# Kernel optimization log

Measured on AMD Instinct MI355X. Metric: run time of the kernel, lower is better.

## Reference

```python
import jax, jax.numpy as jnp
import numpy as np

DIM = 1024
N_QUAT = DIM // 4
LN_EPS = 1e-5
NORM_EPS = 1e-12


def quat_mul(q1, q2):
    # q1, q2: [B, L, N, 4]
    r1, i1, j1, k1 = q1[..., 0], q1[..., 1], q1[..., 2], q1[..., 3]
    r2, i2, j2, k2 = q2[..., 0], q2[..., 1], q2[..., 2], q2[..., 3]
    r = r1 * r2 - i1 * i2 - j1 * j2 - k1 * k2
    i = r1 * i2 + i1 * r2 + j1 * k2 - k1 * j2
    j = r1 * j2 - i1 * k2 + j1 * r2 + k1 * i2
    k = r1 * k2 + i1 * j2 - j1 * i2 + k1 * r2
    return jnp.stack([r, i, j, k], axis=-1)


def quat_conj(q):
    return q * jnp.array([1.0, -1.0, -1.0, -1.0], dtype=q.dtype)


def setup_inputs() -> dict:
    key = jax.random.key(0)
    ks = jax.random.split(key, 7)
    B, L, D = 4, 4096, DIM
    s = 1.0 / np.sqrt(D)
    return {
        "x": jax.random.normal(ks[0], (B, L, D), dtype=jnp.float32),
        "Wk": jax.random.normal(ks[1], (D, D), dtype=jnp.float32) * s,
        "bk": jnp.zeros((D,), dtype=jnp.float32),
        "Wv": jax.random.normal(ks[2], (D, D), dtype=jnp.float32) * s,
        "bv": jnp.zeros((D,), dtype=jnp.float32),
        "ln_g": jnp.ones((D,), dtype=jnp.float32),
        "ln_b": jnp.zeros((D,), dtype=jnp.float32),
        "Wo": jax.random.normal(ks[3], (D, D), dtype=jnp.float32) * s,
        "bo": jnp.zeros((D,), dtype=jnp.float32),
    }


def reference(x, Wk, bk, Wv, bv, ln_g, ln_b, Wo, bo):
    B, L, D = x.shape
    keys = (x @ Wk.T + bk).reshape(B, L, N_QUAT, 4)
    knorm = jnp.linalg.norm(keys, axis=-1, keepdims=True)
    keys = keys / jnp.maximum(knorm, NORM_EPS)  # F.normalize
    values = (x @ Wv.T + bv).reshape(B, L, N_QUAT, 4)
    bound = quat_mul(values, keys)
    memory = jnp.cumsum(bound, axis=1)
    retrieved = quat_mul(memory, quat_conj(keys)).reshape(B, L, D)
    positions = jnp.arange(1, L + 1, dtype=x.dtype)
    retrieved = retrieved / jnp.sqrt(positions)[None, :, None]
    # LayerNorm over last dim
    mu = jnp.mean(retrieved, axis=-1, keepdims=True)
    var = jnp.var(retrieved, axis=-1, keepdims=True)
    normed = (retrieved - mu) / jnp.sqrt(var + LN_EPS) * ln_g + ln_b
    return x + (normed @ Wo.T + bo)
```

## Files before the change

### kernel.cpp

```cpp
#include <hip/hip_runtime.h>
#include <cstdint>
#include <cstddef>


typedef float    f32x4 __attribute__((ext_vector_type(4)));
typedef _Float16 f16x8 __attribute__((ext_vector_type(8)));
typedef _Float16 f16x4 __attribute__((ext_vector_type(4)));

#define DEV static __device__ __forceinline__

constexpr int BATCH = 4;
constexpr int LSEQ  = 4096;
constexpr int DIMN  = 1024;
constexpr int MROW  = BATCH * LSEQ;
constexpr int SEG   = 128;
constexpr int SL    = LSEQ / SEG;
constexpr int NT    = DIMN / 64;

DEV f32x4 qmul(f32x4 a, f32x4 b) {
  f32x4 r;
  r.x = a.x*b.x - a.y*b.y - a.z*b.z - a.w*b.w;
  r.y = a.x*b.y + a.y*b.x + a.z*b.w - a.w*b.z;
  r.z = a.x*b.z - a.y*b.w + a.z*b.x + a.w*b.y;
  r.w = a.x*b.w + a.y*b.z - a.z*b.y + a.w*b.x;
  return r;
}

DEV f32x4 h2f(f16x4 h) {
  return (f32x4){(float)h.x, (float)h.y, (float)h.z, (float)h.w};
}

__global__ __launch_bounds__(256) void k_cast_all(
    const float* __restrict__ x, const float* __restrict__ w0,
    const float* __restrict__ w1, const float* __restrict__ w2,
    _Float16* __restrict__ out) {
  const int XN4 = MROW * DIMN / 4;
  const int WN4 = DIMN * DIMN / 4;
  int i = blockIdx.x * 256 + threadIdx.x;
  if (i >= XN4 + 3 * WN4) return;
  const float* src; int j;
  if (i < XN4)                { src = x;  j = i; }
  else if (i < XN4 + WN4)     { src = w0; j = i - XN4; }
  else if (i < XN4 + 2 * WN4) { src = w1; j = i - XN4 - WN4; }
  else                        { src = w2; j = i - XN4 - 2 * WN4; }
  f32x4 v = ((const f32x4*)src)[j];
  f16x4 o = { (_Float16)v.x, (_Float16)v.y, (_Float16)v.z, (_Float16)v.w };
  ((f16x4*)out)[i] = o;
}

__global__ __launch_bounds__(512, 2) void k_gemm256(
    const _Float16* __restrict__ A, const _Float16* __restrict__ Bw,
    const float* __restrict__ biasA, const float* __restrict__ biasB, int nsplit,
    _Float16* __restrict__ C, int ldC, int nbn) {
  extern __shared__ char smem[];
  const int tid  = threadIdx.x;
  const int lane = tid & 63;
  const int wid  = tid >> 6;
  const int wr = wid >> 2, wc = wid & 3;

  const int nwg = gridDim.x;
  const int cpx = nwg >> 3;
  const int swz = (blockIdx.x & 7) * cpx + (blockIdx.x >> 3);
  const int bm = swz / nbn, bn = swz % nbn;

  auto regBase = [](int slot, int isB, int half) -> unsigned {
    return (unsigned)(((slot * 2 + isB) * 2 + half) * 16384);
  };
  const int r8    = lane >> 3;
  const int sslot = (lane & 7) ^ r8;
  const char* aT = (const char*)(A  + (size_t)bm * 256 * DIMN);
  const char* bT = (const char*)(Bw + (size_t)bn * 256 * DIMN);

  auto stage = [&](int isB, int half, int slot, int kt) {
    const char* gb = (isB ? bT : aT) + (size_t)(half * 128) * 2048 + kt * 128;
    const unsigned reg = regBase(slot, isB, half);
#pragma unroll
    for (int i = 0; i < 2; ++i) {
      const int c = wid * 2 + i;
      const char* src = gb + (size_t)(c * 8 + r8) * 2048 + (sslot << 4);
      __builtin_amdgcn_global_load_lds(
          (const __attribute__((address_space(1))) void*)src,
          (__attribute__((address_space(3))) void*)(smem + reg + c * 1024), 16, 0, 0);
    }
  };
  auto fragA = [&](int slot, int m, int kk) -> f16x8 {
    const int half = m >> 2;
    const int row  = wr * 64 + (m & 3) * 16 + (lane & 15);
    const int sl   = (kk * 4 + (lane >> 4)) ^ (row & 7);
    return *(const f16x8*)(smem + regBase(slot, 0, half) + row * 128 + (sl << 4));
  };
  auto fragB = [&](int slot, int n, int kk) -> f16x8 {
    const int half = n >> 1;
    const int row  = wc * 32 + (n & 1) * 16 + (lane & 15);
    const int sl   = (kk * 4 + (lane >> 4)) ^ (row & 7);
    return *(const f16x8*)(smem + regBase(slot, 1, half) + row * 128 + (sl << 4));
  };

  f32x4 acc[8][4];
#pragma unroll
  for (int m = 0; m < 8; ++m)
#pragma unroll
    for (int n = 0; n < 4; ++n) acc[m][n] = (f32x4){0.f, 0.f, 0.f, 0.f};

  stage(0, 0, 0, 0); stage(0, 1, 0, 0); stage(1, 0, 0, 0); stage(1, 1, 0, 0);

  f16x8 a[4][2], b[4][2];
#pragma unroll 2
  for (int T = 0; T < NT; ++T) {
    const int slot = T & 1, ns = slot ^ 1;
    const bool pf = (T + 1 < NT);
    if (pf) {
      stage(0, 0, ns, T + 1); stage(0, 1, ns, T + 1);
      asm volatile("s_waitcnt vmcnt(4)" ::: "memory");
    } else {
      asm volatile("s_waitcnt vmcnt(0)" ::: "memory");
    }
    __builtin_amdgcn_s_barrier();

#pragma unroll
    for (int m = 0; m < 4; ++m) { a[m][0] = fragA(slot, m, 0); a[m][1] = fragA(slot, m, 1); }
#pragma unroll
    for (int n = 0; n < 4; ++n) { b[n][0] = fragB(slot, n, 0); b[n][1] = fragB(slot, n, 1); }
    __builtin_amdgcn_s_setprio(1);
#pragma unroll
    for (int m = 0; m < 4; ++m)
#pragma unroll
      for (int n = 0; n < 4; ++n) {
        acc[m][n] = __builtin_amdgcn_mfma_f32_16x16x32_f16(a[m][0], b[n][0], acc[m][n], 0, 0, 0);
        acc[m][n] = __builtin_amdgcn_mfma_f32_16x16x32_f16(a[m][1], b[n][1], acc[m][n], 0, 0, 0);
      }
    __builtin_amdgcn_s_setprio(0);

    if (pf) { stage(1, 0, ns, T + 1); stage(1, 1, ns, T + 1); }

#pragma unroll
    for (int m = 0; m < 4; ++m) { a[m][0] = fragA(slot, m + 4, 0); a[m][1] = fragA(slot, m + 4, 1); }
    __builtin_amdgcn_s_setprio(1);
#pragma unroll
    for (int m = 0; m < 4; ++m)
#pragma unroll
      for (int n = 0; n < 4; ++n) {
        acc[m + 4][n] = __builtin_amdgcn_mfma_f32_16x16x32_f16(a[m][0], b[n][0], acc[m + 4][n], 0, 0, 0);
        acc[m + 4][n] = __builtin_amdgcn_mfma_f32_16x16x32_f16(a[m][1], b[n][1], acc[m + 4][n], 0, 0, 0);
      }
    __builtin_amdgcn_s_setprio(0);
    __builtin_amdgcn_s_barrier();
  }

  const int r0 = bm * 256 + wr * 64 + ((lane >> 4) << 2);
  const int c0 = bn * 256 + wc * 32 + (lane & 15);
#pragma unroll
  for (int n = 0; n < 4; ++n) {
    const int col = c0 + (n >> 1) * 128 + (n & 1) * 16;
    const float bc = (col < nsplit) ? biasA[col] : biasB[col - nsplit];
#pragma unroll
    for (int m = 0; m < 8; ++m) {
      const int row = r0 + (m >> 2) * 128 + (m & 3) * 16;
#pragma unroll
      for (int t = 0; t < 4; ++t) {
        C[(size_t)(row + t) * ldC + col] = (_Float16)(acc[m][n][t] + bc);
      }
    }
  }
}

__global__ __launch_bounds__(512, 2) void k_gemm_out(
    const _Float16* __restrict__ A, const _Float16* __restrict__ Bw,
    const float* __restrict__ bias, const _Float16* __restrict__ residH,
    float* __restrict__ C, int nbn) {
  extern __shared__ char smem[];
  const int tid  = threadIdx.x;
  const int lane = tid & 63;
  const int wid  = tid >> 6;
  const int wr = wid >> 2, wc = wid & 3;

  const int nwg = gridDim.x;
  const int cpx = nwg >> 3;
  const int swz = (blockIdx.x & 7) * cpx + (blockIdx.x >> 3);
  const int bm = swz / nbn, bn = swz % nbn;

  const int r8    = lane >> 3;
  const int sslot = (lane & 7) ^ r8;
  const char* aT = (const char*)(A  + (size_t)bm * 128 * DIMN);
  const char* bT = (const char*)(Bw + (size_t)bn * 256 * DIMN);

  auto stage3 = [&](int slot, int kt) {
    char* base = smem + slot * 49152;
#pragma unroll
    for (int i = 0; i < 2; ++i) {
      const int c = wid * 2 + i;
      const char* src = aT + kt * 128 + (size_t)(c * 8 + r8) * 2048 + (sslot << 4);
      __builtin_amdgcn_global_load_lds(
          (const __attribute__((address_space(1))) void*)src,
          (__attribute__((address_space(3))) void*)(base + c * 1024), 16, 0, 0);
    }
#pragma unroll
    for (int i = 0; i < 4; ++i) {
      const int c = wid * 4 + i;
      const char* src = bT + kt * 128 + (size_t)(c * 8 + r8) * 2048 + (sslot << 4);
      __builtin_amdgcn_global_load_lds(
          (const __attribute__((address_space(1))) void*)src,
          (__attribute__((address_space(3))) void*)(base + 16384 + c * 1024), 16, 0, 0);
    }
  };
  auto fragA = [&](int slot, int m, int kk) -> f16x8 {
    const int row = wr * 64 + m * 16 + (lane & 15);
    const int sl  = (kk * 4 + (lane >> 4)) ^ (row & 7);
    return *(const f16x8*)(smem + slot * 49152 + row * 128 + (sl << 4));
  };
  auto fragB = [&](int slot, int n, int kk) -> f16x8 {
    const int row = (n >> 1) * 128 + wc * 32 + (n & 1) * 16 + (lane & 15);
    const int sl  = (kk * 4 + (lane >> 4)) ^ (row & 7);
    return *(const f16x8*)(smem + slot * 49152 + 16384 + row * 128 + (sl << 4));
  };

  f32x4 acc[4][4];
#pragma unroll
  for (int m = 0; m < 4; ++m)
#pragma unroll
    for (int n = 0; n < 4; ++n) acc[m][n] = (f32x4){0.f, 0.f, 0.f, 0.f};

  stage3(0, 0); stage3(1, 1);

  f16x8 a[4][2], b[4][2];
  int s = 0, sw = 2;
  for (int T = 0; T < NT; ++T) {
    if (T + 1 < NT) asm volatile("s_waitcnt vmcnt(6)" ::: "memory");
    else            asm volatile("s_waitcnt vmcnt(0)" ::: "memory");
    __builtin_amdgcn_s_barrier();
#pragma unroll
    for (int m = 0; m < 4; ++m) { a[m][0] = fragA(s, m, 0); a[m][1] = fragA(s, m, 1); }
#pragma unroll
    for (int n = 0; n < 4; ++n) { b[n][0] = fragB(s, n, 0); b[n][1] = fragB(s, n, 1); }
    if (T + 2 < NT) stage3(sw, T + 2);
    __builtin_amdgcn_s_setprio(1);
#pragma unroll
    for (int m = 0; m < 4; ++m)
#pragma unroll
      for (int n = 0; n < 4; ++n) {
        acc[m][n] = __builtin_amdgcn_mfma_f32_16x16x32_f16(a[m][0], b[n][0], acc[m][n], 0, 0, 0);
        acc[m][n] = __builtin_amdgcn_mfma_f32_16x16x32_f16(a[m][1], b[n][1], acc[m][n], 0, 0, 0);
      }
    __builtin_amdgcn_s_setprio(0);
    __builtin_amdgcn_s_barrier();
    s = (s == 2) ? 0 : s + 1;
    sw = (sw == 2) ? 0 : sw + 1;
  }

  const int r0 = bm * 128 + wr * 64 + ((lane >> 4) << 2);
  const int c0 = bn * 256 + wc * 32 + (lane & 15);
#pragma unroll
  for (int n = 0; n < 4; ++n) {
    const int col = c0 + (n >> 1) * 128 + (n & 1) * 16;
    const float bc = bias[col];
#pragma unroll
    for (int m = 0; m < 4; ++m) {
      const int row = r0 + m * 16;
#pragma unroll
      for (int t = 0; t < 4; ++t) {
        const size_t off = (size_t)(row + t) * DIMN + col;
        C[off] = acc[m][n][t] + bc + (float)residH[off];
      }
    }
  }
}

__global__ __launch_bounds__(256) void k_segsum(const _Float16* __restrict__ KVh,
                                                float* __restrict__ segsum) {
  const int b = blockIdx.x >> 7, seg = blockIdx.x & 127, n = threadIdx.x;
  f32x4 ssum = (f32x4){0.f, 0.f, 0.f, 0.f};
  const size_t rb = (size_t)(b * LSEQ + seg * SL) * 2048 + n * 4;
  for (int l = 0; l < SL; ++l) {
    const size_t p = rb + (size_t)l * 2048;
    f32x4 kq = h2f(*(const f16x4*)(KVh + p));
    f32x4 vq = h2f(*(const f16x4*)(KVh + p + 1024));
    float nn = sqrtf(kq.x*kq.x + kq.y*kq.y + kq.z*kq.z + kq.w*kq.w);
    f32x4 kh = kq * (1.0f / fmaxf(nn, 1e-12f));
    ssum += qmul(vq, kh);
  }
  ((f32x4*)segsum)[(size_t)blockIdx.x * 256 + n] = ssum;
}

__global__ __launch_bounds__(256) void k_retrieve_ln(
    const _Float16* __restrict__ KVh, const float* __restrict__ segsum,
    const float* __restrict__ g, const float* __restrict__ bb,
    _Float16* __restrict__ out) {
  const int b = blockIdx.x >> 7, seg = blockIdx.x & 127, n = threadIdx.x;
  const int wid = n >> 6, lane = n & 63;
  __shared__ float p1[2][4], p2[2][4];

  f32x4 m0 = (f32x4){0.f, 0.f, 0.f, 0.f}, m1 = (f32x4){0.f, 0.f, 0.f, 0.f};
  {
    const f32x4* ss = (const f32x4*)segsum + (size_t)b * SEG * 256 + n;
    int s = 0;
    for (; s + 2 <= seg; s += 2) {
      m0 += ss[(size_t)s * 256];
      m1 += ss[(size_t)(s + 1) * 256];
    }
    if (s < seg) m0 += ss[(size_t)s * 256];
  }
  f32x4 mem = m0 + m1;

  const f32x4 gg  = ((const f32x4*)g)[n];
  const f32x4 bvv = ((const f32x4*)bb)[n];
  const size_t rb = (size_t)(b * LSEQ + seg * SL) * 2048 + n * 4;
  const int grow = b * LSEQ + seg * SL;

  f16x4 kq = *(const f16x4*)(KVh + rb);
  f16x4 vq = *(const f16x4*)(KVh + rb + 1024);
  for (int l = 0; l < SL; ++l) {
    f16x4 kqn, vqn;
    if (l + 1 < SL) {
      kqn = *(const f16x4*)(KVh + rb + (size_t)(l + 1) * 2048);
      vqn = *(const f16x4*)(KVh + rb + (size_t)(l + 1) * 2048 + 1024);
    }
    f32x4 kf = h2f(kq), vf = h2f(vq);
    float nn = sqrtf(kf.x*kf.x + kf.y*kf.y + kf.z*kf.z + kf.w*kf.w);
    f32x4 kh = kf * (1.0f / fmaxf(nn, 1e-12f));
    mem += qmul(vf, kh);
    f32x4 kc = (f32x4){kh.x, -kh.y, -kh.z, -kh.w};
    f32x4 r = qmul(mem, kc);
    r *= rsqrtf((float)(seg * SL + l + 1));

    float s1 = r.x + r.y + r.z + r.w;
    float s2 = r.x*r.x + r.y*r.y + r.z*r.z + r.w*r.w;
#pragma unroll
    for (int off = 32; off > 0; off >>= 1) {
      s1 += __shfl_down(s1, off, 64);
      s2 += __shfl_down(s2, off, 64);
    }
    if (lane == 0) { p1[l & 1][wid] = s1; p2[l & 1][wid] = s2; }
    __syncthreads();
    const float ts1 = p1[l & 1][0] + p1[l & 1][1] + p1[l & 1][2] + p1[l & 1][3];
    const float ts2 = p2[l & 1][0] + p2[l & 1][1] + p2[l & 1][2] + p2[l & 1][3];
    const float mu = ts1 * (1.0f / 1024.0f);
    const float var = ts2 * (1.0f / 1024.0f) - mu * mu;
    const float rstd = rsqrtf(var + 1e-5f);
    f32x4 nv = (r - mu) * rstd * gg + bvv;
    f16x4 o = { (_Float16)nv.x, (_Float16)nv.y, (_Float16)nv.z, (_Float16)nv.w };
    ((f16x4*)out)[(size_t)(grow + l) * 256 + n] = o;
    kq = kqn; vq = vqn;
  }
}

extern "C" void kernel_launch(void* const* d_in, const int* in_sizes, int n_in,
                              void* d_out, int out_size, void* d_ws, size_t ws_size,
                              hipStream_t stream) {
  const float* x    = (const float*)d_in[0];
  const float* Wk   = (const float*)d_in[1];
  const float* bk   = (const float*)d_in[2];
  const float* Wv   = (const float*)d_in[3];
  const float* bv   = (const float*)d_in[4];
  const float* ln_g = (const float*)d_in[5];
  const float* ln_b = (const float*)d_in[6];
  const float* Wo   = (const float*)d_in[7];
  const float* bo   = (const float*)d_in[8];
  float* out = (float*)d_out;

  char* ws = (char*)d_ws;
  size_t off = 0;
  auto alloc = [&](size_t bytes) -> void* {
    void* p = ws + off;
    off += (bytes + 255) & ~(size_t)255;
    return p;
  };
  _Float16* xb   = (_Float16*)alloc((size_t)MROW * DIMN * 2);
  _Float16* wkvb = (_Float16*)alloc((size_t)3 * DIMN * DIMN * 2);
  _Float16* KVh  = (_Float16*)alloc((size_t)MROW * 2 * DIMN * 2);
  float* segsum  = (float*)alloc((size_t)BATCH * SEG * DIMN * 4);
  _Float16* nb   = (_Float16*)alloc((size_t)MROW * DIMN * 2);
  _Float16* wob  = wkvb + (size_t)2 * DIMN * DIMN;
  (void)off; (void)ws_size; (void)in_sizes; (void)n_in; (void)out_size;

  hipFuncSetAttribute((const void*)k_gemm256,
                      hipFuncAttributeMaxDynamicSharedMemorySize, 131072);
  hipFuncSetAttribute((const void*)k_gemm_out,
                      hipFuncAttributeMaxDynamicSharedMemorySize, 147456);

  const int castN4 = MROW * DIMN / 4 + 3 * DIMN * DIMN / 4;
  k_cast_all<<<(castN4 + 255) / 256, 256, 0, stream>>>(x, Wk, Wv, Wo, xb);

  k_gemm256<<<(MROW / 256) * (2048 / 256), 512, 131072, stream>>>(
      xb, wkvb, bk, bv, 1024, KVh, 2048, 2048 / 256);

  k_segsum<<<BATCH * SEG, 256, 0, stream>>>(KVh, segsum);
  k_retrieve_ln<<<BATCH * SEG, 256, 0, stream>>>(KVh, segsum, ln_g, ln_b, nb);

  k_gemm_out<<<(MROW / 128) * (DIMN / 256), 512, 147456, stream>>>(
      nb, wob, bo, xb, out, DIMN / 256);
}
```

Baseline: 209.7 us.

## Split GEMM inner loops into quadrant phases interleaving LDS reads, prefetch and MFMA

Both GEMM kernels now run each K tile in smaller MFMA phases over half of the B fragments, ping-ponging between bl and bh registers. LDS fragment reads and global prefetch stages are interleaved between phases, fenced by extra barriers and lgkmcnt waits. The aim is to overlap LDS and global latency with matrix-core work and to cut register pressure from holding all B fragments at once. The cost is more barriers per iteration, and a full vmcnt(0) drain inside the first kernel's loop may serialise the prefetch it was meant to hide.

```diff
diff --git a/kernel.cpp b/kernel.cpp
--- a/kernel.cpp
+++ b/kernel.cpp
@@ -103,45 +103,73 @@
     for (int n = 0; n < 4; ++n) acc[m][n] = (f32x4){0.f, 0.f, 0.f, 0.f};
 
   stage(0, 0, 0, 0); stage(0, 1, 0, 0); stage(1, 0, 0, 0); stage(1, 1, 0, 0);
-
-  f16x8 a[4][2], b[4][2];
+  asm volatile("s_waitcnt vmcnt(0)" ::: "memory");
+  __builtin_amdgcn_s_barrier();
+
+  f16x8 a[4][2], bl[2][2], bh[2][2];
 #pragma unroll 2
   for (int T = 0; T < NT; ++T) {
     const int slot = T & 1, ns = slot ^ 1;
     const bool pf = (T + 1 < NT);
-    if (pf) {
-      stage(0, 0, ns, T + 1); stage(0, 1, ns, T + 1);
-      asm volatile("s_waitcnt vmcnt(4)" ::: "memory");
-    } else {
-      asm volatile("s_waitcnt vmcnt(0)" ::: "memory");
-    }
-    __builtin_amdgcn_s_barrier();
 
 #pragma unroll
     for (int m = 0; m < 4; ++m) { a[m][0] = fragA(slot, m, 0); a[m][1] = fragA(slot, m, 1); }
 #pragma unroll
-    for (int n = 0; n < 4; ++n) { b[n][0] = fragB(slot, n, 0); b[n][1] = fragB(slot, n, 1); }
-    __builtin_amdgcn_s_setprio(1);
-#pragma unroll
-    for (int m = 0; m < 4; ++m)
-#pragma unroll
-      for (int n = 0; n < 4; ++n) {
-        acc[m][n] = __builtin_amdgcn_mfma_f32_16x16x32_f16(a[m][0], b[n][0], acc[m][n], 0, 0, 0);
-        acc[m][n] = __builtin_amdgcn_mfma_f32_16x16x32_f16(a[m][1], b[n][1], acc[m][n], 0, 0, 0);
-      }
-    __builtin_amdgcn_s_setprio(0);
-
+    for (int n = 0; n < 2; ++n) { bl[n][0] = fragB(slot, n, 0); bl[n][1] = fragB(slot, n, 1); }
+    if (pf) { stage(0, 0, ns, T + 1); stage(0, 1, ns, T + 1); }
+    __builtin_amdgcn_s_barrier();
+    asm volatile("s_waitcnt lgkmcnt(0)" ::: "memory");
+    __builtin_amdgcn_s_setprio(1);
+#pragma unroll
+    for (int m = 0; m < 4; ++m)
+#pragma unroll
+      for (int n = 0; n < 2; ++n) {
+        acc[m][n] = __builtin_amdgcn_mfma_f32_16x16x32_f16(a[m][0], bl[n][0], acc[m][n], 0, 0, 0);
+        acc[m][n] = __builtin_amdgcn_mfma_f32_16x16x32_f16(a[m][1], bl[n][1], acc[m][n], 0, 0, 0);
+      }
+    __builtin_amdgcn_s_setprio(0);
+    __builtin_amdgcn_s_barrier();
+
+#pragma unroll
+    for (int n = 0; n < 2; ++n) { bh[n][0] = fragB(slot, n + 2, 0); bh[n][1] = fragB(slot, n + 2, 1); }
     if (pf) { stage(1, 0, ns, T + 1); stage(1, 1, ns, T + 1); }
+    __builtin_amdgcn_s_barrier();
+    asm volatile("s_waitcnt lgkmcnt(0)" ::: "memory");
+    __builtin_amdgcn_s_setprio(1);
+#pragma unroll
+    for (int m = 0; m < 4; ++m)
+#pragma unroll
+      for (int n = 0; n < 2; ++n) {
+        acc[m][n + 2] = __builtin_amdgcn_mfma_f32_16x16x32_f16(a[m][0], bh[n][0], acc[m][n + 2], 0, 0, 0);
+        acc[m][n + 2] = __builtin_amdgcn_mfma_f32_16x16x32_f16(a[m][1], bh[n][1], acc[m][n + 2], 0, 0, 0);
+      }
+    __builtin_amdgcn_s_setprio(0);
+    __builtin_amdgcn_s_barrier();
 
 #pragma unroll
     for (int m = 0; m < 4; ++m) { a[m][0] = fragA(slot, m + 4, 0); a[m][1] = fragA(slot, m + 4, 1); }
-    __builtin_amdgcn_s_setprio(1);
-#pragma unroll
-    for (int m = 0; m < 4; ++m)
-#pragma unroll
-      for (int n = 0; n < 4; ++n) {
-        acc[m + 4][n] = __builtin_amdgcn_mfma_f32_16x16x32_f16(a[m][0], b[n][0], acc[m + 4][n], 0, 0, 0);
-        acc[m + 4][n] = __builtin_amdgcn_mfma_f32_16x16x32_f16(a[m][1], b[n][1], acc[m + 4][n], 0, 0, 0);
+    __builtin_amdgcn_s_barrier();
+    asm volatile("s_waitcnt lgkmcnt(0)" ::: "memory");
+    __builtin_amdgcn_s_setprio(1);
+#pragma unroll
+    for (int m = 0; m < 4; ++m)
+#pragma unroll
+      for (int n = 0; n < 2; ++n) {
+        acc[m + 4][n + 2] = __builtin_amdgcn_mfma_f32_16x16x32_f16(a[m][0], bh[n][0], acc[m + 4][n + 2], 0, 0, 0);
+        acc[m + 4][n + 2] = __builtin_amdgcn_mfma_f32_16x16x32_f16(a[m][1], bh[n][1], acc[m + 4][n + 2], 0, 0, 0);
+      }
+    __builtin_amdgcn_s_setprio(0);
+    __builtin_amdgcn_s_barrier();
+
+    asm volatile("s_waitcnt vmcnt(0)" ::: "memory");
+    __builtin_amdgcn_s_barrier();
+    __builtin_amdgcn_s_setprio(1);
+#pragma unroll
+    for (int m = 0; m < 4; ++m)
+#pragma unroll
+      for (int n = 0; n < 2; ++n) {
+        acc[m + 4][n] = __builtin_amdgcn_mfma_f32_16x16x32_f16(a[m][0], bl[n][0], acc[m + 4][n], 0, 0, 0);
+        acc[m + 4][n] = __builtin_amdgcn_mfma_f32_16x16x32_f16(a[m][1], bl[n][1], acc[m + 4][n], 0, 0, 0);
       }
     __builtin_amdgcn_s_setprio(0);
     __builtin_amdgcn_s_barrier();
@@ -221,25 +249,42 @@
     for (int n = 0; n < 4; ++n) acc[m][n] = (f32x4){0.f, 0.f, 0.f, 0.f};
 
   stage3(0, 0); stage3(1, 1);
-
-  f16x8 a[4][2], b[4][2];
+  asm volatile("s_waitcnt vmcnt(6)" ::: "memory");
+  __builtin_amdgcn_s_barrier();
+
+  f16x8 a[4][2], bl[2][2], bh[2][2];
   int s = 0, sw = 2;
   for (int T = 0; T < NT; ++T) {
-    if (T + 1 < NT) asm volatile("s_waitcnt vmcnt(6)" ::: "memory");
+#pragma unroll
+    for (int m = 0; m < 4; ++m) { a[m][0] = fragA(s, m, 0); a[m][1] = fragA(s, m, 1); }
+#pragma unroll
+    for (int n = 0; n < 2; ++n) { bl[n][0] = fragB(s, n, 0); bl[n][1] = fragB(s, n, 1); }
+    if (T + 2 < NT) stage3(sw, T + 2);
+    __builtin_amdgcn_s_barrier();
+    asm volatile("s_waitcnt lgkmcnt(0)" ::: "memory");
+    __builtin_amdgcn_s_setprio(1);
+#pragma unroll
+    for (int m = 0; m < 4; ++m)
+#pragma unroll
+      for (int n = 0; n < 2; ++n) {
+        acc[m][n] = __builtin_amdgcn_mfma_f32_16x16x32_f16(a[m][0], bl[n][0], acc[m][n], 0, 0, 0);
+        acc[m][n] = __builtin_amdgcn_mfma_f32_16x16x32_f16(a[m][1], bl[n][1], acc[m][n], 0, 0, 0);
+      }
+    __builtin_amdgcn_s_setprio(0);
+    __builtin_amdgcn_s_barrier();
+#pragma unroll
+    for (int n = 0; n < 2; ++n) { bh[n][0] = fragB(s, n + 2, 0); bh[n][1] = fragB(s, n + 2, 1); }
+    if (T + 2 < NT) asm volatile("s_waitcnt vmcnt(6)" ::: "memory");
     else            asm volatile("s_waitcnt vmcnt(0)" ::: "memory");
     __builtin_amdgcn_s_barrier();
-#pragma unroll
-    for (int m = 0; m < 4; ++m) { a[m][0] = fragA(s, m, 0); a[m][1] = fragA(s, m, 1); }
-#pragma unroll
-    for (int n = 0; n < 4; ++n) { b[n][0] = fragB(s, n, 0); b[n][1] = fragB(s, n, 1); }
-    if (T + 2 < NT) stage3(sw, T + 2);
-    __builtin_amdgcn_s_setprio(1);
-#pragma unroll
-    for (int m = 0; m < 4; ++m)
-#pragma unroll
-      for (int n = 0; n < 4; ++n) {
-        acc[m][n] = __builtin_amdgcn_mfma_f32_16x16x32_f16(a[m][0], b[n][0], acc[m][n], 0, 0, 0);
-        acc[m][n] = __builtin_amdgcn_mfma_f32_16x16x32_f16(a[m][1], b[n][1], acc[m][n], 0, 0, 0);
+    asm volatile("s_waitcnt lgkmcnt(0)" ::: "memory");
+    __builtin_amdgcn_s_setprio(1);
+#pragma unroll
+    for (int m = 0; m < 4; ++m)
+#pragma unroll
+      for (int n = 0; n < 2; ++n) {
+        acc[m][n + 2] = __builtin_amdgcn_mfma_f32_16x16x32_f16(a[m][0], bh[n][0], acc[m][n + 2], 0, 0, 0);
+        acc[m][n + 2] = __builtin_amdgcn_mfma_f32_16x16x32_f16(a[m][1], bh[n][1], acc[m][n + 2], 0, 0, 0);
       }
     __builtin_amdgcn_s_setprio(0);
     __builtin_amdgcn_s_barrier();
```

Result: no change. 210.2 us (+0.3%).

## Fuse x fp16 cast into KV GEMM and use 256x256 tiles for output GEMM

Applied to the files above, without the earlier changes.

The KV projection GEMM now reads x in fp32 straight from global memory into registers, converts to fp16 and writes the swizzled tile to LDS itself. This removes the separate cast pass over x and its fp16 copy, and the output GEMM adds the fp32 residual x directly. The output GEMM moves from a 128x256 triple-buffered tile to a 256x256 double-buffered tile, and both GEMMs now interleave A-fragment loads with MFMAs in smaller chunks. In exchange, A staging uses registers and explicit LDS writes instead of direct global-to-LDS loads. The output GEMM also waits on all loads each iteration, which may expose memory latency.

```diff
diff --git a/kernel.cpp b/kernel.cpp
--- a/kernel.cpp
+++ b/kernel.cpp
@@ -30,28 +30,32 @@
   return (f32x4){(float)h.x, (float)h.y, (float)h.z, (float)h.w};
 }
 
-__global__ __launch_bounds__(256) void k_cast_all(
-    const float* __restrict__ x, const float* __restrict__ w0,
-    const float* __restrict__ w1, const float* __restrict__ w2,
-    _Float16* __restrict__ out) {
-  const int XN4 = MROW * DIMN / 4;
+DEV f16x8 cvt8(f32x4 lo, f32x4 hi) {
+  f16x8 r;
+  r[0] = (_Float16)lo.x; r[1] = (_Float16)lo.y; r[2] = (_Float16)lo.z; r[3] = (_Float16)lo.w;
+  r[4] = (_Float16)hi.x; r[5] = (_Float16)hi.y; r[6] = (_Float16)hi.z; r[7] = (_Float16)hi.w;
+  return r;
+}
+
+__global__ __launch_bounds__(256) void k_cast_w(
+    const float* __restrict__ w0, const float* __restrict__ w1,
+    const float* __restrict__ w2, _Float16* __restrict__ out) {
   const int WN4 = DIMN * DIMN / 4;
   int i = blockIdx.x * 256 + threadIdx.x;
-  if (i >= XN4 + 3 * WN4) return;
+  if (i >= 3 * WN4) return;
   const float* src; int j;
-  if (i < XN4)                { src = x;  j = i; }
-  else if (i < XN4 + WN4)     { src = w0; j = i - XN4; }
-  else if (i < XN4 + 2 * WN4) { src = w1; j = i - XN4 - WN4; }
-  else                        { src = w2; j = i - XN4 - 2 * WN4; }
+  if (i < WN4)          { src = w0; j = i; }
+  else if (i < 2 * WN4) { src = w1; j = i - WN4; }
+  else                  { src = w2; j = i - 2 * WN4; }
   f32x4 v = ((const f32x4*)src)[j];
   f16x4 o = { (_Float16)v.x, (_Float16)v.y, (_Float16)v.z, (_Float16)v.w };
   ((f16x4*)out)[i] = o;
 }
 
-__global__ __launch_bounds__(512, 2) void k_gemm256(
-    const _Float16* __restrict__ A, const _Float16* __restrict__ Bw,
-    const float* __restrict__ biasA, const float* __restrict__ biasB, int nsplit,
-    _Float16* __restrict__ C, int ldC, int nbn) {
+__global__ __launch_bounds__(512, 2) void k_gemm_kv(
+    const float* __restrict__ X, const _Float16* __restrict__ Bw,
+    const float* __restrict__ biasA, const float* __restrict__ biasB,
+    _Float16* __restrict__ C) {
   extern __shared__ char smem[];
   const int tid  = threadIdx.x;
   const int lane = tid & 63;
@@ -61,19 +65,19 @@
   const int nwg = gridDim.x;
   const int cpx = nwg >> 3;
   const int swz = (blockIdx.x & 7) * cpx + (blockIdx.x >> 3);
-  const int bm = swz / nbn, bn = swz % nbn;
+  const int bm = swz >> 3, bn = swz & 7;
+
+  const int r8    = lane >> 3;
+  const int sslot = (lane & 7) ^ r8;
+  const float* aX = X + (size_t)bm * 256 * DIMN;
+  const char* bT  = (const char*)(Bw + (size_t)bn * 256 * DIMN);
 
   auto regBase = [](int slot, int isB, int half) -> unsigned {
     return (unsigned)(((slot * 2 + isB) * 2 + half) * 16384);
   };
-  const int r8    = lane >> 3;
-  const int sslot = (lane & 7) ^ r8;
-  const char* aT = (const char*)(A  + (size_t)bm * 256 * DIMN);
-  const char* bT = (const char*)(Bw + (size_t)bn * 256 * DIMN);
-
-  auto stage = [&](int isB, int half, int slot, int kt) {
-    const char* gb = (isB ? bT : aT) + (size_t)(half * 128) * 2048 + kt * 128;
-    const unsigned reg = regBase(slot, isB, half);
+  auto stageB = [&](int half, int slot, int kt) {
+    const char* gb = bT + (size_t)(half * 128) * 2048 + kt * 128;
+    const unsigned reg = regBase(slot, 1, half);
 #pragma unroll
     for (int i = 0; i < 2; ++i) {
       const int c = wid * 2 + i;
@@ -83,6 +87,27 @@
           (__attribute__((address_space(3))) void*)(smem + reg + c * 1024), 16, 0, 0);
     }
   };
+  f32x4 areg[4][2];
+  auto loadA = [&](int kt) {
+#pragma unroll
+    for (int h = 0; h < 2; ++h)
+#pragma unroll
+      for (int i = 0; i < 2; ++i) {
+        const size_t ad = (size_t)(h * 128 + (wid * 2 + i) * 8 + r8) * DIMN
+                        + kt * 64 + sslot * 8;
+        areg[h * 2 + i][0] = *(const f32x4*)(aX + ad);
+        areg[h * 2 + i][1] = *(const f32x4*)(aX + ad + 4);
+      }
+  };
+  auto writeA = [&](int slot) {
+#pragma unroll
+    for (int h = 0; h < 2; ++h)
+#pragma unroll
+      for (int i = 0; i < 2; ++i) {
+        f16x8 v = cvt8(areg[h * 2 + i][0], areg[h * 2 + i][1]);
+        *(f16x8*)(smem + regBase(slot, 0, h) + (wid * 2 + i) * 1024 + lane * 16) = v;
+      }
+  };
   auto fragA = [&](int slot, int m, int kk) -> f16x8 {
     const int half = m >> 2;
     const int row  = wr * 64 + (m & 3) * 16 + (lane & 15);
@@ -102,49 +127,50 @@
 #pragma unroll
     for (int n = 0; n < 4; ++n) acc[m][n] = (f32x4){0.f, 0.f, 0.f, 0.f};
 
-  stage(0, 0, 0, 0); stage(0, 1, 0, 0); stage(1, 0, 0, 0); stage(1, 1, 0, 0);
-
-  f16x8 a[4][2], b[4][2];
+  loadA(0);
+  stageB(0, 0, 0); stageB(1, 0, 0);
+  asm volatile("s_waitcnt vmcnt(4)" ::: "memory");
+  __builtin_amdgcn_sched_barrier(0);
+  writeA(0);
+
 #pragma unroll 2
   for (int T = 0; T < NT; ++T) {
     const int slot = T & 1, ns = slot ^ 1;
     const bool pf = (T + 1 < NT);
     if (pf) {
-      stage(0, 0, ns, T + 1); stage(0, 1, ns, T + 1);
-      asm volatile("s_waitcnt vmcnt(4)" ::: "memory");
+      loadA(T + 1);
+      asm volatile("s_waitcnt vmcnt(8)" ::: "memory");
     } else {
       asm volatile("s_waitcnt vmcnt(0)" ::: "memory");
     }
+    asm volatile("s_waitcnt lgkmcnt(0)" ::: "memory");
     __builtin_amdgcn_s_barrier();
 
-#pragma unroll
-    for (int m = 0; m < 4; ++m) { a[m][0] = fragA(slot, m, 0); a[m][1] = fragA(slot, m, 1); }
+    f16x8 b[4][2], a2[2][2];
 #pragma unroll
     for (int n = 0; n < 4; ++n) { b[n][0] = fragB(slot, n, 0); b[n][1] = fragB(slot, n, 1); }
-    __builtin_amdgcn_s_setprio(1);
-#pragma unroll
-    for (int m = 0; m < 4; ++m)
-#pragma unroll
-      for (int n = 0; n < 4; ++n) {
-        acc[m][n] = __builtin_amdgcn_mfma_f32_16x16x32_f16(a[m][0], b[n][0], acc[m][n], 0, 0, 0);
-        acc[m][n] = __builtin_amdgcn_mfma_f32_16x16x32_f16(a[m][1], b[n][1], acc[m][n], 0, 0, 0);
-      }
-    __builtin_amdgcn_s_setprio(0);
-
-    if (pf) { stage(1, 0, ns, T + 1); stage(1, 1, ns, T + 1); }
-
-#pragma unroll
-    for (int m = 0; m < 4; ++m) { a[m][0] = fragA(slot, m + 4, 0); a[m][1] = fragA(slot, m + 4, 1); }
-    __builtin_amdgcn_s_setprio(1);
-#pragma unroll
-    for (int m = 0; m < 4; ++m)
-#pragma unroll
-      for (int n = 0; n < 4; ++n) {
-        acc[m + 4][n] = __builtin_amdgcn_mfma_f32_16x16x32_f16(a[m][0], b[n][0], acc[m + 4][n], 0, 0, 0);
-        acc[m + 4][n] = __builtin_amdgcn_mfma_f32_16x16x32_f16(a[m][1], b[n][1], acc[m + 4][n], 0, 0, 0);
-      }
-    __builtin_amdgcn_s_setprio(0);
-    __builtin_amdgcn_s_barrier();
+    if (pf) { stageB(0, ns, T + 1); stageB(1, ns, T + 1); }
+
+#pragma unroll
+    for (int mh = 0; mh < 4; ++mh) {
+      a2[0][0] = fragA(slot, mh * 2, 0);     a2[0][1] = fragA(slot, mh * 2, 1);
+      a2[1][0] = fragA(slot, mh * 2 + 1, 0); a2[1][1] = fragA(slot, mh * 2 + 1, 1);
+      __builtin_amdgcn_s_setprio(1);
+#pragma unroll
+      for (int mm = 0; mm < 2; ++mm)
+#pragma unroll
+        for (int n = 0; n < 4; ++n) {
+          acc[mh*2+mm][n] = __builtin_amdgcn_mfma_f32_16x16x32_f16(a2[mm][0], b[n][0], acc[mh*2+mm][n], 0, 0, 0);
+          acc[mh*2+mm][n] = __builtin_amdgcn_mfma_f32_16x16x32_f16(a2[mm][1], b[n][1], acc[mh*2+mm][n], 0, 0, 0);
+        }
+      __builtin_amdgcn_s_setprio(0);
+    }
+
+    if (pf) {
+      asm volatile("s_waitcnt vmcnt(4)" ::: "memory");
+      __builtin_amdgcn_sched_barrier(0);
+      writeA(ns);
+    }
   }
 
   const int r0 = bm * 256 + wr * 64 + ((lane >> 4) << 2);
@@ -152,13 +178,13 @@
 #pragma unroll
   for (int n = 0; n < 4; ++n) {
     const int col = c0 + (n >> 1) * 128 + (n & 1) * 16;
-    const float bc = (col < nsplit) ? biasA[col] : biasB[col - nsplit];
+    const float bc = (col < DIMN) ? biasA[col] : biasB[col - DIMN];
 #pragma unroll
     for (int m = 0; m < 8; ++m) {
       const int row = r0 + (m >> 2) * 128 + (m & 3) * 16;
 #pragma unroll
       for (int t = 0; t < 4; ++t) {
-        C[(size_t)(row + t) * ldC + col] = (_Float16)(acc[m][n][t] + bc);
+        C[(size_t)(row + t) * 2048 + col] = (_Float16)(acc[m][n][t] + bc);
       }
     }
   }
@@ -166,8 +192,8 @@
 
 __global__ __launch_bounds__(512, 2) void k_gemm_out(
     const _Float16* __restrict__ A, const _Float16* __restrict__ Bw,
-    const float* __restrict__ bias, const _Float16* __restrict__ residH,
-    float* __restrict__ C, int nbn) {
+    const float* __restrict__ bias, const float* __restrict__ resid,
+    float* __restrict__ C) {
   extern __shared__ char smem[];
   const int tid  = threadIdx.x;
   const int lane = tid & 63;
@@ -177,89 +203,92 @@
   const int nwg = gridDim.x;
   const int cpx = nwg >> 3;
   const int swz = (blockIdx.x & 7) * cpx + (blockIdx.x >> 3);
-  const int bm = swz / nbn, bn = swz % nbn;
+  const int bm = swz >> 2, bn = swz & 3;
 
   const int r8    = lane >> 3;
   const int sslot = (lane & 7) ^ r8;
-  const char* aT = (const char*)(A  + (size_t)bm * 128 * DIMN);
+  const char* aT = (const char*)(A  + (size_t)bm * 256 * DIMN);
   const char* bT = (const char*)(Bw + (size_t)bn * 256 * DIMN);
 
-  auto stage3 = [&](int slot, int kt) {
-    char* base = smem + slot * 49152;
+  auto regBase = [](int slot, int isB, int half) -> unsigned {
+    return (unsigned)(((slot * 2 + isB) * 2 + half) * 16384);
+  };
+  auto stage = [&](int isB, int half, int slot, int kt) {
+    const char* gb = (isB ? bT : aT) + (size_t)(half * 128) * 2048 + kt * 128;
+    const unsigned reg = regBase(slot, isB, half);
 #pragma unroll
     for (int i = 0; i < 2; ++i) {
       const int c = wid * 2 + i;
-      const char* src = aT + kt * 128 + (size_t)(c * 8 + r8) * 2048 + (sslot << 4);
+      const char* src = gb + (size_t)(c * 8 + r8) * 2048 + (sslot << 4);
       __builtin_amdgcn_global_load_lds(
           (const __attribute__((address_space(1))) void*)src,
-          (__attribute__((address_space(3))) void*)(base + c * 1024), 16, 0, 0);
-    }
-#pragma unroll
-    for (int i = 0; i < 4; ++i) {
-      const int c = wid * 4 + i;
-      const char* src = bT + kt * 128 + (size_t)(c * 8 + r8) * 2048 + (sslot << 4);
-      __builtin_amdgcn_global_load_lds(
-          (const __attribute__((address_space(1))) void*)src,
-          (__attribute__((address_space(3))) void*)(base + 16384 + c * 1024), 16, 0, 0);
+          (__attribute__((address_space(3))) void*)(smem + reg + c * 1024), 16, 0, 0);
     }
   };
   auto fragA = [&](int slot, int m, int kk) -> f16x8 {
-    const int row = wr * 64 + m * 16 + (lane & 15);
-    const int sl  = (kk * 4 + (lane >> 4)) ^ (row & 7);
-    return *(const f16x8*)(smem + slot * 49152 + row * 128 + (sl << 4));
+    const int half = m >> 2;
+    const int row  = wr * 64 + (m & 3) * 16 + (lane & 15);
+    const int sl   = (kk * 4 + (lane >> 4)) ^ (row & 7);
+    return *(const f16x8*)(smem + regBase(slot, 0, half) + row * 128 + (sl << 4));
   };
   auto fragB = [&](int slot, int n, int kk) -> f16x8 {
-    const int row = (n >> 1) * 128 + wc * 32 + (n & 1) * 16 + (lane & 15);
-    const int sl  = (kk * 4 + (lane >> 4)) ^ (row & 7);
-    return *(const f16x8*)(smem + slot * 49152 + 16384 + row * 128 + (sl << 4));
-  };
-
-  f32x4 acc[4][4];
-#pragma unroll
-  for (int m = 0; m < 4; ++m)
+    const int half = n >> 1;
+    const int row  = wc * 32 + (n & 1) * 16 + (lane & 15);
+    const int sl   = (kk * 4 + (lane >> 4)) ^ (row & 7);
+    return *(const f16x8*)(smem + regBase(slot, 1, half) + row * 128 + (sl << 4));
+  };
+
+  f32x4 acc[8][4];
+#pragma unroll
+  for (int m = 0; m < 8; ++m)
 #pragma unroll
     for (int n = 0; n < 4; ++n) acc[m][n] = (f32x4){0.f, 0.f, 0.f, 0.f};
 
-  stage3(0, 0); stage3(1, 1);
-
-  f16x8 a[4][2], b[4][2];
-  int s = 0, sw = 2;
+  stage(0, 0, 0, 0); stage(0, 1, 0, 0); stage(1, 0, 0, 0); stage(1, 1, 0, 0);
+
+#pragma unroll 2
   for (int T = 0; T < NT; ++T) {
-    if (T + 1 < NT) asm volatile("s_waitcnt vmcnt(6)" ::: "memory");
-    else            asm volatile("s_waitcnt vmcnt(0)" ::: "memory");
+    const int slot = T & 1, ns = slot ^ 1;
+    const bool pf = (T + 1 < NT);
+    asm volatile("s_waitcnt vmcnt(0)" ::: "memory");
     __builtin_amdgcn_s_barrier();
-#pragma unroll
-    for (int m = 0; m < 4; ++m) { a[m][0] = fragA(s, m, 0); a[m][1] = fragA(s, m, 1); }
-#pragma unroll
-    for (int n = 0; n < 4; ++n) { b[n][0] = fragB(s, n, 0); b[n][1] = fragB(s, n, 1); }
-    if (T + 2 < NT) stage3(sw, T + 2);
-    __builtin_amdgcn_s_setprio(1);
-#pragma unroll
-    for (int m = 0; m < 4; ++m)
-#pragma unroll
-      for (int n = 0; n < 4; ++n) {
-        acc[m][n] = __builtin_amdgcn_mfma_f32_16x16x32_f16(a[m][0], b[n][0], acc[m][n], 0, 0, 0);
-        acc[m][n] = __builtin_amdgcn_mfma_f32_16x16x32_f16(a[m][1], b[n][1], acc[m][n], 0, 0, 0);
-      }
-    __builtin_amdgcn_s_setprio(0);
-    __builtin_amdgcn_s_barrier();
-    s = (s == 2) ? 0 : s + 1;
-    sw = (sw == 2) ? 0 : sw + 1;
-  }
-
-  const int r0 = bm * 128 + wr * 64 + ((lane >> 4) << 2);
+
+    f16x8 b[4][2], a2[2][2];
+#pragma unroll
+    for (int n = 0; n < 4; ++n) { b[n][0] = fragB(slot, n, 0); b[n][1] = fragB(slot, n, 1); }
+    if (pf) {
+      stage(0, 0, ns, T + 1); stage(0, 1, ns, T + 1);
+      stage(1, 0, ns, T + 1); stage(1, 1, ns, T + 1);
+    }
+#pragma unroll
+    for (int mh = 0; mh < 4; ++mh) {
+      a2[0][0] = fragA(slot, mh * 2, 0);     a2[0][1] = fragA(slot, mh * 2, 1);
+      a2[1][0] = fragA(slot, mh * 2 + 1, 0); a2[1][1] = fragA(slot, mh * 2 + 1, 1);
+      __builtin_amdgcn_s_setprio(1);
+#pragma unroll
+      for (int mm = 0; mm < 2; ++mm)
+#pragma unroll
+        for (int n = 0; n < 4; ++n) {
+          acc[mh*2+mm][n] = __builtin_amdgcn_mfma_f32_16x16x32_f16(a2[mm][0], b[n][0], acc[mh*2+mm][n], 0, 0, 0);
+          acc[mh*2+mm][n] = __builtin_amdgcn_mfma_f32_16x16x32_f16(a2[mm][1], b[n][1], acc[mh*2+mm][n], 0, 0, 0);
+        }
+      __builtin_amdgcn_s_setprio(0);
+    }
+  }
+
+  const int r0 = bm * 256 + wr * 64 + ((lane >> 4) << 2);
   const int c0 = bn * 256 + wc * 32 + (lane & 15);
 #pragma unroll
   for (int n = 0; n < 4; ++n) {
     const int col = c0 + (n >> 1) * 128 + (n & 1) * 16;
     const float bc = bias[col];
 #pragma unroll
-    for (int m = 0; m < 4; ++m) {
-      const int row = r0 + m * 16;
+    for (int m = 0; m < 8; ++m) {
+      const int row = r0 + (m >> 2) * 128 + (m & 3) * 16;
 #pragma unroll
       for (int t = 0; t < 4; ++t) {
         const size_t off = (size_t)(row + t) * DIMN + col;
-        C[off] = acc[m][n][t] + bc + (float)residH[off];
+        C[off] = acc[m][n][t] + bc + resid[off];
       }
     }
   }
@@ -364,7 +393,6 @@
     off += (bytes + 255) & ~(size_t)255;
     return p;
   };
-  _Float16* xb   = (_Float16*)alloc((size_t)MROW * DIMN * 2);
   _Float16* wkvb = (_Float16*)alloc((size_t)3 * DIMN * DIMN * 2);
   _Float16* KVh  = (_Float16*)alloc((size_t)MROW * 2 * DIMN * 2);
   float* segsum  = (float*)alloc((size_t)BATCH * SEG * DIMN * 4);
@@ -372,20 +400,19 @@
   _Float16* wob  = wkvb + (size_t)2 * DIMN * DIMN;
   (void)off; (void)ws_size; (void)in_sizes; (void)n_in; (void)out_size;
 
-  hipFuncSetAttribute((const void*)k_gemm256,
+  hipFuncSetAttribute((const void*)k_gemm_kv,
                       hipFuncAttributeMaxDynamicSharedMemorySize, 131072);
   hipFuncSetAttribute((const void*)k_gemm_out,
-                      hipFuncAttributeMaxDynamicSharedMemorySize, 147456);
-
-  const int castN4 = MROW * DIMN / 4 + 3 * DIMN * DIMN / 4;
-  k_cast_all<<<(castN4 + 255) / 256, 256, 0, stream>>>(x, Wk, Wv, Wo, xb);
-
-  k_gemm256<<<(MROW / 256) * (2048 / 256), 512, 131072, stream>>>(
-      xb, wkvb, bk, bv, 1024, KVh, 2048, 2048 / 256);
+                      hipFuncAttributeMaxDynamicSharedMemorySize, 131072);
+
+  k_cast_w<<<(3 * DIMN * DIMN / 4 + 255) / 256, 256, 0, stream>>>(Wk, Wv, Wo, wkvb);
+
+  k_gemm_kv<<<(MROW / 256) * (2048 / 256), 512, 131072, stream>>>(
+      x, wkvb, bk, bv, KVh);
 
   k_segsum<<<BATCH * SEG, 256, 0, stream>>>(KVh, segsum);
   k_retrieve_ln<<<BATCH * SEG, 256, 0, stream>>>(KVh, segsum, ln_g, ln_b, nb);
 
-  k_gemm_out<<<(MROW / 128) * (DIMN / 256), 512, 147456, stream>>>(
-      nb, wob, bo, xb, out, DIMN / 256);
-}
+  k_gemm_out<<<(MROW / 256) * (DIMN / 256), 512, 131072, stream>>>(
+      nb, wob, bo, x, out);
+}
```

New measurement: 225.8 us. 1.08x slower.

## Shrink output GEMM tile to 128x128 with 4 waves and double buffering

Applied to the files above, without the earlier changes.

The output projection GEMM changes from 128x256 tiles with 8 waves and a triple-buffered LDS pipeline to 128x128 tiles with 4 waves and double buffering in 64KB of LDS. The grid doubles to 1024 workgroups, which gives better CU fill and lets more workgroups share a CU. Each wave keeps the same 64x64 register tile. The trade-off is more global traffic for A reloads, since each A tile is now read by twice as many workgroups, and a shallower prefetch pipeline that can expose load latency.

```diff
diff --git a/kernel.cpp b/kernel.cpp
--- a/kernel.cpp
+++ b/kernel.cpp
@@ -164,54 +164,47 @@
   }
 }
 
-__global__ __launch_bounds__(512, 2) void k_gemm_out(
+__global__ __launch_bounds__(256, 2) void k_gemm_out(
     const _Float16* __restrict__ A, const _Float16* __restrict__ Bw,
     const float* __restrict__ bias, const _Float16* __restrict__ residH,
-    float* __restrict__ C, int nbn) {
+    float* __restrict__ C) {
   extern __shared__ char smem[];
   const int tid  = threadIdx.x;
   const int lane = tid & 63;
   const int wid  = tid >> 6;
-  const int wr = wid >> 2, wc = wid & 3;
+  const int wr = wid >> 1, wc = wid & 1;
 
   const int nwg = gridDim.x;
   const int cpx = nwg >> 3;
   const int swz = (blockIdx.x & 7) * cpx + (blockIdx.x >> 3);
-  const int bm = swz / nbn, bn = swz % nbn;
+  const int bm = swz >> 3, bn = swz & 7;
 
   const int r8    = lane >> 3;
   const int sslot = (lane & 7) ^ r8;
   const char* aT = (const char*)(A  + (size_t)bm * 128 * DIMN);
-  const char* bT = (const char*)(Bw + (size_t)bn * 256 * DIMN);
-
-  auto stage3 = [&](int slot, int kt) {
-    char* base = smem + slot * 49152;
-#pragma unroll
-    for (int i = 0; i < 2; ++i) {
-      const int c = wid * 2 + i;
-      const char* src = aT + kt * 128 + (size_t)(c * 8 + r8) * 2048 + (sslot << 4);
+  const char* bT = (const char*)(Bw + (size_t)bn * 128 * DIMN);
+
+  auto stage = [&](int isB, int slot, int kt) {
+    const char* gb = (isB ? bT : aT) + kt * 128;
+    char* dst = smem + slot * 32768 + isB * 16384;
+#pragma unroll
+    for (int i = 0; i < 4; ++i) {
+      const int c = wid * 4 + i;
+      const char* src = gb + (size_t)(c * 8 + r8) * 2048 + (sslot << 4);
       __builtin_amdgcn_global_load_lds(
           (const __attribute__((address_space(1))) void*)src,
-          (__attribute__((address_space(3))) void*)(base + c * 1024), 16, 0, 0);
-    }
-#pragma unroll
-    for (int i = 0; i < 4; ++i) {
-      const int c = wid * 4 + i;
-      const char* src = bT + kt * 128 + (size_t)(c * 8 + r8) * 2048 + (sslot << 4);
-      __builtin_amdgcn_global_load_lds(
-          (const __attribute__((address_space(1))) void*)src,
-          (__attribute__((address_space(3))) void*)(base + 16384 + c * 1024), 16, 0, 0);
+          (__attribute__((address_space(3))) void*)(dst + c * 1024), 16, 0, 0);
     }
   };
   auto fragA = [&](int slot, int m, int kk) -> f16x8 {
     const int row = wr * 64 + m * 16 + (lane & 15);
     const int sl  = (kk * 4 + (lane >> 4)) ^ (row & 7);
-    return *(const f16x8*)(smem + slot * 49152 + row * 128 + (sl << 4));
+    return *(const f16x8*)(smem + slot * 32768 + row * 128 + (sl << 4));
   };
   auto fragB = [&](int slot, int n, int kk) -> f16x8 {
-    const int row = (n >> 1) * 128 + wc * 32 + (n & 1) * 16 + (lane & 15);
+    const int row = wc * 64 + n * 16 + (lane & 15);
     const int sl  = (kk * 4 + (lane >> 4)) ^ (row & 7);
-    return *(const f16x8*)(smem + slot * 49152 + 16384 + row * 128 + (sl << 4));
+    return *(const f16x8*)(smem + slot * 32768 + 16384 + row * 128 + (sl << 4));
   };
 
   f32x4 acc[4][4];
@@ -220,19 +213,25 @@
 #pragma unroll
     for (int n = 0; n < 4; ++n) acc[m][n] = (f32x4){0.f, 0.f, 0.f, 0.f};
 
-  stage3(0, 0); stage3(1, 1);
+  stage(0, 0, 0); stage(1, 0, 0);
 
   f16x8 a[4][2], b[4][2];
-  int s = 0, sw = 2;
+#pragma unroll 2
   for (int T = 0; T < NT; ++T) {
-    if (T + 1 < NT) asm volatile("s_waitcnt vmcnt(6)" ::: "memory");
-    else            asm volatile("s_waitcnt vmcnt(0)" ::: "memory");
+    const int slot = T & 1, ns = slot ^ 1;
+    const bool pf = (T + 1 < NT);
+    if (pf) {
+      stage(0, ns, T + 1);
+      asm volatile("s_waitcnt vmcnt(4)" ::: "memory");
+    } else {
+      asm volatile("s_waitcnt vmcnt(0)" ::: "memory");
+    }
     __builtin_amdgcn_s_barrier();
 #pragma unroll
-    for (int m = 0; m < 4; ++m) { a[m][0] = fragA(s, m, 0); a[m][1] = fragA(s, m, 1); }
-#pragma unroll
-    for (int n = 0; n < 4; ++n) { b[n][0] = fragB(s, n, 0); b[n][1] = fragB(s, n, 1); }
-    if (T + 2 < NT) stage3(sw, T + 2);
+    for (int m = 0; m < 4; ++m) { a[m][0] = fragA(slot, m, 0); a[m][1] = fragA(slot, m, 1); }
+#pragma unroll
+    for (int n = 0; n < 4; ++n) { b[n][0] = fragB(slot, n, 0); b[n][1] = fragB(slot, n, 1); }
+    if (pf) stage(1, ns, T + 1);
     __builtin_amdgcn_s_setprio(1);
 #pragma unroll
     for (int m = 0; m < 4; ++m)
@@ -243,15 +242,13 @@
       }
     __builtin_amdgcn_s_setprio(0);
     __builtin_amdgcn_s_barrier();
-    s = (s == 2) ? 0 : s + 1;
-    sw = (sw == 2) ? 0 : sw + 1;
   }
 
   const int r0 = bm * 128 + wr * 64 + ((lane >> 4) << 2);
-  const int c0 = bn * 256 + wc * 32 + (lane & 15);
+  const int c0 = bn * 128 + wc * 64 + (lane & 15);
 #pragma unroll
   for (int n = 0; n < 4; ++n) {
-    const int col = c0 + (n >> 1) * 128 + (n & 1) * 16;
+    const int col = c0 + n * 16;
     const float bc = bias[col];
 #pragma unroll
     for (int m = 0; m < 4; ++m) {
@@ -375,7 +372,7 @@
   hipFuncSetAttribute((const void*)k_gemm256,
                       hipFuncAttributeMaxDynamicSharedMemorySize, 131072);
   hipFuncSetAttribute((const void*)k_gemm_out,
-                      hipFuncAttributeMaxDynamicSharedMemorySize, 147456);
+                      hipFuncAttributeMaxDynamicSharedMemorySize, 65536);
 
   const int castN4 = MROW * DIMN / 4 + 3 * DIMN * DIMN / 4;
   k_cast_all<<<(castN4 + 255) / 256, 256, 0, stream>>>(x, Wk, Wv, Wo, xb);
@@ -386,6 +383,6 @@
   k_segsum<<<BATCH * SEG, 256, 0, stream>>>(KVh, segsum);
   k_retrieve_ln<<<BATCH * SEG, 256, 0, stream>>>(KVh, segsum, ln_g, ln_b, nb);
 
-  k_gemm_out<<<(MROW / 128) * (DIMN / 256), 512, 147456, stream>>>(
-      nb, wob, bo, xb, out, DIMN / 256);
-}
+  k_gemm_out<<<(MROW / 128) * (DIMN / 128), 256, 65536, stream>>>(
+      nb, wob, bo, xb, out);
+}
```

Result: no change. 208.4 us (-0.6%).
